# Performance work log

Hardware: AMD Instinct MI355X
Metric: run time of the kernel (lower is better)

The kernel has to match this reference:

```python
import jax, jax.numpy as jnp
import numpy as np

NUM_HEADS = 8
NUM_UNITS = 512


def setup_inputs() -> dict:
    key = jax.random.key(0)
    ks = jax.random.split(key, 5)
    B, S, D = 2, 4096, NUM_UNITS
    scale = 1.0 / np.sqrt(D)
    return {
        "x": jax.random.normal(ks[0], (B, S, D), dtype=jnp.float32),
        "Wq": jax.random.normal(ks[1], (D, NUM_UNITS), dtype=jnp.float32) * scale,
        "Wk": jax.random.normal(ks[2], (D, NUM_UNITS), dtype=jnp.float32) * scale,
        "Wv": jax.random.normal(ks[3], (D, NUM_UNITS), dtype=jnp.float32) * scale,
        "Wo": jax.random.normal(ks[4], (D, NUM_UNITS), dtype=jnp.float32) * scale,
    }


def reference(x, Wq, Wk, Wv, Wo):
    B, S, _ = x.shape
    H = NUM_HEADS
    Dh = NUM_UNITS // H

    # QKV linear projections (self-attention: K_V = (x, x))
    Q = x @ Wq  # [B,S,U]
    K = x @ Wk
    V = x @ Wv

    # split heads -> [B,H,S,Dh]
    def split(t):
        return t.reshape(B, S, H, Dh).transpose(0, 2, 1, 3)

    Qh, Kh, Vh = split(Q), split(K), split(V)

    # scaled dot-product attention, bias = 0, no mask, no dropout (training=False)
    scores = jnp.einsum("bhqd,bhkd->bhqk", Qh, Kh) / jnp.sqrt(
        jnp.asarray(Dh, dtype=x.dtype)
    )
    attn = jax.nn.softmax(scores, axis=-1)
    ctx = jnp.einsum("bhqk,bhkd->bhqd", attn, Vh)

    # combine heads -> [B,S,U], then output projection
    ctx = ctx.transpose(0, 2, 1, 3).reshape(B, S, NUM_UNITS)
    return ctx @ Wo
```

## Files before the change

kernel.cpp:

```cpp
#include <hip/hip_runtime.h>

typedef __attribute__((ext_vector_type(8))) short short8;
typedef __attribute__((ext_vector_type(4))) float f32x4;
typedef __attribute__((ext_vector_type(4))) unsigned short us4;
typedef unsigned short ushort_t;
typedef unsigned int uint_t;

typedef const __attribute__((address_space(1))) void* gas1;
typedef __attribute__((address_space(3))) void* las3;

#define LDS_FENCE()                                            \
  do {                                                         \
    asm volatile("s_waitcnt lgkmcnt(0)" ::: "memory");         \
    __builtin_amdgcn_sched_barrier(0);                         \
  } while (0)

__device__ __forceinline__ ushort_t f2b(float f) {
  union { float f; uint_t u; } v; v.f = f;
  return (ushort_t)((v.u + 0x7fffu + ((v.u >> 16) & 1u)) >> 16);
}

__device__ __forceinline__ uint_t cvtpk(float lo, float hi) {
  uint_t r;
  asm("v_cvt_pk_bf16_f32 %0, %1, %2" : "=v"(r) : "v"(lo), "v"(hi));
  return r;
}

__device__ __forceinline__ void gld_lds16(const ushort_t* g, void* l) {
  __builtin_amdgcn_global_load_lds((gas1)g, (las3)l, 16, 0, 0);
}

__global__ void cvt_x_kernel(const float* __restrict__ x, ushort_t* __restrict__ xb, int n4) {
  int i = blockIdx.x * blockDim.x + threadIdx.x;
  if (i >= n4) return;
  float4 v = ((const float4*)x)[i];
  ushort4 o;
  o.x = f2b(v.x); o.y = f2b(v.y); o.z = f2b(v.z); o.w = f2b(v.w);
  ((ushort4*)xb)[i] = o;
}

__global__ void cvt_wt_kernel(const float* __restrict__ W0, const float* __restrict__ W1,
                              const float* __restrict__ W2, const float* __restrict__ W3,
                              ushort_t* __restrict__ T0, ushort_t* __restrict__ T1,
                              ushort_t* __restrict__ T2, ushort_t* __restrict__ T3) {
  const float* W; ushort_t* T;
  switch (blockIdx.z) {
    case 0: W = W0; T = T0; break;
    case 1: W = W1; T = T1; break;
    case 2: W = W2; T = T2; break;
    default: W = W3; T = T3; break;
  }
  __shared__ ushort_t Tl[64 * 68];
  int t = threadIdx.x;
  int kt = blockIdx.x & 7, nt = blockIdx.x >> 3;
  int krow = t >> 4;
  int ncol = (t & 15) * 4;
#pragma unroll
  for (int j = 0; j < 4; ++j) {
    int k = j * 16 + krow;
    float4 v = *(const float4*)&W[(size_t)(kt * 64 + k) * 512 + nt * 64 + ncol];
    const float* vf = (const float*)&v;
#pragma unroll
    for (int e = 0; e < 4; ++e)
      Tl[(ncol + e) * 68 + k] = f2b(vf[e]);
  }
  __syncthreads();
#pragma unroll
  for (int j = 0; j < 4; ++j) {
    int f = j * 1024 + t * 4;
    int n = f >> 6, k = f & 63;
    *(ushort4*)&T[(size_t)(nt * 64 + n) * 512 + kt * 64 + k] =
        *(const ushort4*)&Tl[n * 68 + k];
  }
}

__global__ __launch_bounds__(256) void gemm_qkv_kernel(
    const ushort_t* __restrict__ A,
    const ushort_t* __restrict__ WqT, const ushort_t* __restrict__ WkT,
    const ushort_t* __restrict__ WvT,
    ushort_t* __restrict__ Qo, ushort_t* __restrict__ Ko, ushort_t* __restrict__ VTo) {
  const int K = 512, N = 512, S = 4096;
  const ushort_t* BT; ushort_t* out; int mode;
  switch (blockIdx.z) {
    case 0: BT = WqT; out = Qo;  mode = 0; break;
    case 1: BT = WkT; out = Ko;  mode = 0; break;
    default: BT = WvT; out = VTo; mode = 1; break;
  }
  __shared__ ushort_t Al[128 * 64];
  __shared__ ushort_t Bl[128 * 64];

  int tid = threadIdx.x, lane = tid & 63, w = tid >> 6;
  int g = lane >> 4, ln = lane & 15;
  int wr = w >> 1, wc = w & 1;
  int m0 = blockIdx.y * 128;
  int n0 = blockIdx.x * 128;

  f32x4 acc[4][4];
  const f32x4 zz = {0.f, 0.f, 0.f, 0.f};
#pragma unroll
  for (int i = 0; i < 4; ++i)
#pragma unroll
    for (int j = 0; j < 4; ++j) acc[i][j] = zz;

  for (int kt = 0; kt < 8; ++kt) {
    __syncthreads();
#pragma unroll
    for (int i = 0; i < 4; ++i) {
      int p = i * 256 + tid, row = p >> 3, sl = p & 7, sp = sl ^ (row & 7);
      gld_lds16(A + (size_t)(m0 + row) * K + kt * 64 + sp * 8,
                (char*)Al + (i * 256 + (tid & 192)) * 16);
    }
#pragma unroll
    for (int i = 0; i < 4; ++i) {
      int p = i * 256 + tid, row = p >> 3, sl = p & 7, sp = sl ^ (row & 7);
      gld_lds16(BT + (size_t)(n0 + row) * K + kt * 64 + sp * 8,
                (char*)Bl + (i * 256 + (tid & 192)) * 16);
    }
    __syncthreads();

#pragma unroll
    for (int kc = 0; kc < 2; ++kc) {
      short8 af[4], bf[4];
#pragma unroll
      for (int mt = 0; mt < 4; ++mt) {
        int row = wr * 64 + mt * 16 + ln;
        af[mt] = *(const short8*)((char*)Al + row * 128 + (((kc * 4 + g) ^ (row & 7)) * 16));
      }
#pragma unroll
      for (int nt = 0; nt < 4; ++nt) {
        int row = wc * 64 + nt * 16 + ln;
        bf[nt] = *(const short8*)((char*)Bl + row * 128 + (((kc * 4 + g) ^ (row & 7)) * 16));
      }
#pragma unroll
      for (int mt = 0; mt < 4; ++mt)
#pragma unroll
        for (int nt = 0; nt < 4; ++nt)
          acc[mt][nt] = __builtin_amdgcn_mfma_f32_16x16x32_bf16(af[mt], bf[nt], acc[mt][nt], 0, 0, 0);
    }
  }

  if (mode == 0) {
#pragma unroll
    for (int mt = 0; mt < 4; ++mt)
#pragma unroll
      for (int nt = 0; nt < 4; ++nt)
#pragma unroll
        for (int jj = 0; jj < 4; ++jj) {
          int m = m0 + wr * 64 + mt * 16 + 4 * g + jj;
          int n = n0 + wc * 64 + nt * 16 + ln;
          out[(size_t)m * N + n] = f2b(acc[mt][nt][jj]);
        }
  } else {
#pragma unroll
    for (int mt = 0; mt < 4; ++mt)
#pragma unroll
      for (int nt = 0; nt < 4; ++nt) {
        int s0 = m0 + wr * 64 + mt * 16 + 4 * g;
        int u = n0 + wc * 64 + nt * 16 + ln;
        int b = s0 >> 12, s = s0 & 4095;
        int h = u >> 6, d = u & 63;
        us4 pv;
#pragma unroll
        for (int jj = 0; jj < 4; ++jj) pv[jj] = f2b(acc[mt][nt][jj]);
        *(us4*)&VTo[((size_t)((b * 8 + h) * 64 + d)) * S + s] = pv;
      }
  }
}

__global__ __launch_bounds__(256) void gemm_ao_kernel(
    const ushort_t* __restrict__ A, const ushort_t* __restrict__ BT,
    float* __restrict__ out) {
  const int K = 512, N = 512;
  __shared__ ushort_t Al[128 * 64];
  __shared__ ushort_t Bl[128 * 64];

  int tid = threadIdx.x, lane = tid & 63, w = tid >> 6;
  int g = lane >> 4, ln = lane & 15;
  int wr = w >> 1, wc = w & 1;
  int m0 = blockIdx.y * 128;
  int n0 = blockIdx.x * 128;

  f32x4 acc[4][4];
  const f32x4 zz = {0.f, 0.f, 0.f, 0.f};
#pragma unroll
  for (int i = 0; i < 4; ++i)
#pragma unroll
    for (int j = 0; j < 4; ++j) acc[i][j] = zz;

  for (int kt = 0; kt < 8; ++kt) {
    __syncthreads();
#pragma unroll
    for (int i = 0; i < 4; ++i) {
      int p = i * 256 + tid, row = p >> 3, sl = p & 7, sp = sl ^ (row & 7);
      gld_lds16(A + (size_t)(m0 + row) * K + kt * 64 + sp * 8,
                (char*)Al + (i * 256 + (tid & 192)) * 16);
    }
#pragma unroll
    for (int i = 0; i < 4; ++i) {
      int p = i * 256 + tid, row = p >> 3, sl = p & 7, sp = sl ^ (row & 7);
      gld_lds16(BT + (size_t)(n0 + row) * K + kt * 64 + sp * 8,
                (char*)Bl + (i * 256 + (tid & 192)) * 16);
    }
    __syncthreads();

#pragma unroll
    for (int kc = 0; kc < 2; ++kc) {
      short8 af[4], bf[4];
#pragma unroll
      for (int mt = 0; mt < 4; ++mt) {
        int row = wr * 64 + mt * 16 + ln;
        af[mt] = *(const short8*)((char*)Al + row * 128 + (((kc * 4 + g) ^ (row & 7)) * 16));
      }
#pragma unroll
      for (int nt = 0; nt < 4; ++nt) {
        int row = wc * 64 + nt * 16 + ln;
        bf[nt] = *(const short8*)((char*)Bl + row * 128 + (((kc * 4 + g) ^ (row & 7)) * 16));
      }
#pragma unroll
      for (int mt = 0; mt < 4; ++mt)
#pragma unroll
        for (int nt = 0; nt < 4; ++nt)
          acc[mt][nt] = __builtin_amdgcn_mfma_f32_16x16x32_bf16(af[mt], bf[nt], acc[mt][nt], 0, 0, 0);
    }
  }
#pragma unroll
  for (int mt = 0; mt < 4; ++mt)
#pragma unroll
    for (int nt = 0; nt < 4; ++nt)
#pragma unroll
      for (int jj = 0; jj < 4; ++jj) {
        int m = m0 + wr * 64 + mt * 16 + 4 * g + jj;
        int n = n0 + wc * 64 + nt * 16 + ln;
        out[(size_t)m * N + n] = acc[mt][nt][jj];
      }
}

__global__ __launch_bounds__(256) void attn_kernel(
    const ushort_t* __restrict__ Qg, const ushort_t* __restrict__ Kg,
    const ushort_t* __restrict__ VTg, ushort_t* __restrict__ CTXg) {
  const int S = 4096, U = 512, DH = 64;
  const float CSC = 0.125f * 1.44269504089f;
  int qb = blockIdx.x, h = blockIdx.y, b = blockIdx.z;
  int tid = threadIdx.x, lane = tid & 63, w = tid >> 6;
  int g = lane >> 4, ln = lane & 15;

  __shared__ ushort_t Kl[64 * 64];
  __shared__ ushort_t Vl[64 * 64];
  __shared__ ushort_t Pl[4][16 * 72];

  const ushort_t* qp = Qg + ((size_t)b * S + qb * 64 + w * 16 + ln) * U + h * DH + g * 8;
  short8 qf0 = *(const short8*)qp;
  short8 qf1 = *(const short8*)(qp + 32);

  f32x4 acc[4];
  const f32x4 zz = {0.f, 0.f, 0.f, 0.f};
#pragma unroll
  for (int i = 0; i < 4; ++i) acc[i] = zz;
  float mrun = -INFINITY, lrun = 0.f;

  int r = tid >> 3;
  int c8 = (tid & 7) * 8;
  const ushort_t* kbase = Kg + ((size_t)b * S + r) * U + h * DH + c8;
  const ushort_t* vbase = VTg + ((size_t)((b * 8 + h) * 64 + r)) * S + c8;

  for (int it = 0; it < 64; ++it) {
    int kv0 = it * 64;
    uint4 k1 = *(const uint4*)(kbase + (size_t)kv0 * U);
    uint4 k2 = *(const uint4*)(kbase + (size_t)(kv0 + 32) * U);
    uint4 v1 = *(const uint4*)(vbase + kv0);
    uint4 v2 = *(const uint4*)(vbase + (size_t)32 * S + kv0);
    __syncthreads();
    {
      int by1 = (r * 128 + c8 * 2) ^ ((r & 7) << 4);
      *(uint4*)((char*)Kl + by1) = k1;
      *(uint4*)((char*)Vl + by1) = v1;
      int r2 = r + 32;
      int by2 = (r2 * 128 + c8 * 2) ^ ((r2 & 7) << 4);
      *(uint4*)((char*)Kl + by2) = k2;
      *(uint4*)((char*)Vl + by2) = v2;
    }
    __syncthreads();

    f32x4 st[4];
#pragma unroll
    for (int m = 0; m < 4; ++m) {
      int row = m * 16 + ln;
      short8 kf0 = *(const short8*)((char*)Kl + ((row * 128 + 16 * g) ^ ((row & 7) << 4)));
      short8 kf1 = *(const short8*)((char*)Kl + ((row * 128 + 64 + 16 * g) ^ ((row & 7) << 4)));
      st[m] = __builtin_amdgcn_mfma_f32_16x16x32_bf16(kf0, qf0, zz, 0, 0, 0);
      st[m] = __builtin_amdgcn_mfma_f32_16x16x32_bf16(kf1, qf1, st[m], 0, 0, 0);
    }

    float mx0 = fmaxf(fmaxf(st[0][0], st[0][1]), fmaxf(st[0][2], st[0][3]));
    float mx1 = fmaxf(fmaxf(st[1][0], st[1][1]), fmaxf(st[1][2], st[1][3]));
    float mx2 = fmaxf(fmaxf(st[2][0], st[2][1]), fmaxf(st[2][2], st[2][3]));
    float mx3 = fmaxf(fmaxf(st[3][0], st[3][1]), fmaxf(st[3][2], st[3][3]));
    float smax = fmaxf(fmaxf(mx0, mx1), fmaxf(mx2, mx3));
    smax = fmaxf(smax, __shfl_xor(smax, 16));
    smax = fmaxf(smax, __shfl_xor(smax, 32));
    float tmax = smax * CSC;

    float mnew = fmaxf(mrun, tmax);
    if (!__all(tmax <= mrun + 8.0f)) {
      float alpha = __builtin_amdgcn_exp2f(mrun - mnew);
      mrun = mnew;
      lrun *= alpha;
      float av[4];
#pragma unroll
      for (int jj = 0; jj < 4; ++jj) av[jj] = __shfl(alpha, 4 * g + jj);
#pragma unroll
      for (int dt = 0; dt < 4; ++dt)
#pragma unroll
        for (int jj = 0; jj < 4; ++jj) acc[dt][jj] *= av[jj];
    }

    float nb = -mrun;
    float p[16];
    float ps = 0.f;
#pragma unroll
    for (int m = 0; m < 4; ++m)
#pragma unroll
      for (int jj = 0; jj < 4; ++jj) {
        float y = __builtin_amdgcn_exp2f(__builtin_fmaf(st[m][jj], CSC, nb));
        p[m * 4 + jj] = y;
        ps += y;
      }
    ps += __shfl_xor(ps, 16);
    ps += __shfl_xor(ps, 32);
    lrun += ps;

#pragma unroll
    for (int m = 0; m < 4; ++m) {
      uint2 pv;
      pv.x = cvtpk(p[m * 4 + 0], p[m * 4 + 1]);
      pv.y = cvtpk(p[m * 4 + 2], p[m * 4 + 3]);
      *(uint2*)&Pl[w][ln * 72 + m * 16 + 4 * g] = pv;
    }
    LDS_FENCE();

#pragma unroll
    for (int c = 0; c < 2; ++c) {
      short8 pf = *(const short8*)&Pl[w][ln * 72 + 32 * c + 8 * g];
#pragma unroll
      for (int dt = 0; dt < 4; ++dt) {
        int row = dt * 16 + ln;
        short8 vf = *(const short8*)((char*)Vl + ((row * 128 + 64 * c + 16 * g) ^ ((row & 7) << 4)));
        acc[dt] = __builtin_amdgcn_mfma_f32_16x16x32_bf16(pf, vf, acc[dt], 0, 0, 0);
      }
    }
  }

  float inv_l = 1.f / lrun;
  float lv[4];
#pragma unroll
  for (int jj = 0; jj < 4; ++jj) lv[jj] = __shfl(inv_l, 4 * g + jj);
#pragma unroll
  for (int dt = 0; dt < 4; ++dt)
#pragma unroll
    for (int jj = 0; jj < 4; ++jj) {
      int s = qb * 64 + w * 16 + 4 * g + jj;
      int u = h * 64 + dt * 16 + ln;
      CTXg[((size_t)b * S + s) * U + u] = f2b(acc[dt][jj] * lv[jj]);
    }
}

extern "C" void kernel_launch(void* const* d_in, const int* in_sizes, int n_in,
                              void* d_out, int out_size, void* d_ws, size_t ws_size,
                              hipStream_t stream) {
  const float* x  = (const float*)d_in[0];
  const float* Wq = (const float*)d_in[1];
  const float* Wk = (const float*)d_in[2];
  const float* Wv = (const float*)d_in[3];
  const float* Wo = (const float*)d_in[4];
  float* out = (float*)d_out;

  ushort_t* ws  = (ushort_t*)d_ws;
  ushort_t* xb  = ws;
  ushort_t* WqT = xb + 4194304;
  ushort_t* WkT = WqT + 262144;
  ushort_t* WvT = WkT + 262144;
  ushort_t* WoT = WvT + 262144;
  ushort_t* Qb  = WoT + 262144;
  ushort_t* Kb  = Qb + 4194304;
  ushort_t* VTb = Kb + 4194304;
  ushort_t* CTX = xb;

  cvt_x_kernel<<<4096, 256, 0, stream>>>(x, xb, 1048576);
  cvt_wt_kernel<<<dim3(64, 1, 4), 256, 0, stream>>>(Wq, Wk, Wv, Wo, WqT, WkT, WvT, WoT);
  gemm_qkv_kernel<<<dim3(4, 64, 3), 256, 0, stream>>>(xb, WqT, WkT, WvT, Qb, Kb, VTb);
  attn_kernel<<<dim3(64, 8, 2), 256, 0, stream>>>(Qb, Kb, VTb, CTX);
  gemm_ao_kernel<<<dim3(4, 64), 256, 0, stream>>>(CTX, WoT, out);
}
```

Measured before the change: 250.0 us.

## Split attention KV range across two blocks and merge partials in a combine kernel

The attention kernel now splits the key/value sequence into parts (two when workspace allows), with each block handling half the KV tiles. Each block writes a normalized partial output plus a log-sum-exp value, and a new combine kernel merges the partials into the context buffer. This doubles the grid from 1024 to 2048 blocks to raise occupancy on a GPU with many CUs, at the cost of an extra kernel launch, extra partial-output traffic, and an extra bf16 rounding of the partials. The row-max reduction is also regrouped into three-input max operations.

```diff
diff --git a/kernel.cpp b/kernel.cpp
--- a/kernel.cpp
+++ b/kernel.cpp
@@ -20,6 +20,11 @@
   return (ushort_t)((v.u + 0x7fffu + ((v.u >> 16) & 1u)) >> 16);
 }
 
+__device__ __forceinline__ float b2f(ushort_t u) {
+  union { uint_t u; float f; } v; v.u = ((uint_t)u) << 16;
+  return v.f;
+}
+
 __device__ __forceinline__ uint_t cvtpk(float lo, float hi) {
   uint_t r;
   asm("v_cvt_pk_bf16_f32 %0, %1, %2" : "=v"(r) : "v"(lo), "v"(hi));
@@ -28,6 +33,10 @@
 
 __device__ __forceinline__ void gld_lds16(const ushort_t* g, void* l) {
   __builtin_amdgcn_global_load_lds((gas1)g, (las3)l, 16, 0, 0);
+}
+
+__device__ __forceinline__ float max3f(float a, float b, float c) {
+  return fmaxf(fmaxf(a, b), c);
 }
 
 __global__ void cvt_x_kernel(const float* __restrict__ x, ushort_t* __restrict__ xb, int n4) {
@@ -237,10 +246,13 @@
 
 __global__ __launch_bounds__(256) void attn_kernel(
     const ushort_t* __restrict__ Qg, const ushort_t* __restrict__ Kg,
-    const ushort_t* __restrict__ VTg, ushort_t* __restrict__ CTXg) {
+    const ushort_t* __restrict__ VTg, ushort_t* __restrict__ Obuf,
+    float* __restrict__ Lbuf, int ntiles) {
   const int S = 4096, U = 512, DH = 64;
   const float CSC = 0.125f * 1.44269504089f;
-  int qb = blockIdx.x, h = blockIdx.y, b = blockIdx.z;
+  int qb = blockIdx.x, h = blockIdx.y;
+  int b = blockIdx.z & 1, part = blockIdx.z >> 1;
+  int bh = b * 8 + h;
   int tid = threadIdx.x, lane = tid & 63, w = tid >> 6;
   int g = lane >> 4, ln = lane & 15;
 
@@ -261,10 +273,11 @@
   int r = tid >> 3;
   int c8 = (tid & 7) * 8;
   const ushort_t* kbase = Kg + ((size_t)b * S + r) * U + h * DH + c8;
-  const ushort_t* vbase = VTg + ((size_t)((b * 8 + h) * 64 + r)) * S + c8;
-
-  for (int it = 0; it < 64; ++it) {
-    int kv0 = it * 64;
+  const ushort_t* vbase = VTg + ((size_t)(bh * 64 + r)) * S + c8;
+
+  int it0 = part * ntiles;
+  for (int ii = 0; ii < ntiles; ++ii) {
+    int kv0 = (it0 + ii) * 64;
     uint4 k1 = *(const uint4*)(kbase + (size_t)kv0 * U);
     uint4 k2 = *(const uint4*)(kbase + (size_t)(kv0 + 32) * U);
     uint4 v1 = *(const uint4*)(vbase + kv0);
@@ -291,11 +304,12 @@
       st[m] = __builtin_amdgcn_mfma_f32_16x16x32_bf16(kf1, qf1, st[m], 0, 0, 0);
     }
 
-    float mx0 = fmaxf(fmaxf(st[0][0], st[0][1]), fmaxf(st[0][2], st[0][3]));
-    float mx1 = fmaxf(fmaxf(st[1][0], st[1][1]), fmaxf(st[1][2], st[1][3]));
-    float mx2 = fmaxf(fmaxf(st[2][0], st[2][1]), fmaxf(st[2][2], st[2][3]));
-    float mx3 = fmaxf(fmaxf(st[3][0], st[3][1]), fmaxf(st[3][2], st[3][3]));
-    float smax = fmaxf(fmaxf(mx0, mx1), fmaxf(mx2, mx3));
+    float t0 = max3f(st[0][0], st[0][1], st[0][2]);
+    float t1 = max3f(st[0][3], st[1][0], st[1][1]);
+    float t2 = max3f(st[1][2], st[1][3], st[2][0]);
+    float t3 = max3f(st[2][1], st[2][2], st[2][3]);
+    float t4 = max3f(st[3][0], st[3][1], st[3][2]);
+    float smax = fmaxf(max3f(t0, t1, t2), max3f(t3, t4, st[3][3]));
     smax = fmaxf(smax, __shfl_xor(smax, 16));
     smax = fmaxf(smax, __shfl_xor(smax, 32));
     float tmax = smax * CSC;
@@ -354,14 +368,58 @@
   float lv[4];
 #pragma unroll
   for (int jj = 0; jj < 4; ++jj) lv[jj] = __shfl(inv_l, 4 * g + jj);
+  ushort_t* ob = Obuf + (size_t)part * 4194304 + ((size_t)bh * S) * 64;
 #pragma unroll
   for (int dt = 0; dt < 4; ++dt)
 #pragma unroll
     for (int jj = 0; jj < 4; ++jj) {
       int s = qb * 64 + w * 16 + 4 * g + jj;
-      int u = h * 64 + dt * 16 + ln;
-      CTXg[((size_t)b * S + s) * U + u] = f2b(acc[dt][jj] * lv[jj]);
-    }
+      int d = dt * 16 + ln;
+      ob[(size_t)s * 64 + d] = f2b(acc[dt][jj] * lv[jj]);
+    }
+  if (g == 0) {
+    int s = qb * 64 + w * 16 + ln;
+    Lbuf[part * 65536 + bh * S + s] = mrun + __log2f(lrun);
+  }
+}
+
+__global__ void combine_kernel(const ushort_t* __restrict__ Obuf,
+                               const float* __restrict__ Lbuf,
+                               ushort_t* __restrict__ CTX, int nparts) {
+  int tid = threadIdx.x;
+  int row = blockIdx.x * 32 + (tid >> 3);
+  int c = (tid & 7) * 8;
+  int bh = row >> 12, s = row & 4095;
+  int b = bh >> 3, h = bh & 7;
+
+  us4 n0a = *(const us4*)&Obuf[(size_t)row * 64 + c];
+  us4 n0b = *(const us4*)&Obuf[(size_t)row * 64 + c + 4];
+  float o[8];
+  if (nparts == 2) {
+    float L0 = Lbuf[row];
+    float L1 = Lbuf[65536 + row];
+    us4 n1a = *(const us4*)&Obuf[(size_t)(4194304 + row * 64) + c];
+    us4 n1b = *(const us4*)&Obuf[(size_t)(4194304 + row * 64) + c + 4];
+    float Lm = fmaxf(L0, L1);
+    float w0 = __builtin_amdgcn_exp2f(L0 - Lm);
+    float w1 = __builtin_amdgcn_exp2f(L1 - Lm);
+    float inv = 1.f / (w0 + w1);
+    float a0 = w0 * inv, a1 = w1 * inv;
+#pragma unroll
+    for (int j = 0; j < 4; ++j) {
+      o[j]     = a0 * b2f(n0a[j]) + a1 * b2f(n1a[j]);
+      o[j + 4] = a0 * b2f(n0b[j]) + a1 * b2f(n1b[j]);
+    }
+  } else {
+#pragma unroll
+    for (int j = 0; j < 4; ++j) { o[j] = b2f(n0a[j]); o[j + 4] = b2f(n0b[j]); }
+  }
+  us4 w0v, w1v;
+#pragma unroll
+  for (int j = 0; j < 4; ++j) { w0v[j] = f2b(o[j]); w1v[j] = f2b(o[j + 4]); }
+  ushort_t* dst = &CTX[((size_t)(b * 4096 + s)) * 512 + h * 64 + c];
+  *(us4*)dst = w0v;
+  *(us4*)(dst + 4) = w1v;
 }
 
 extern "C" void kernel_launch(void* const* d_in, const int* in_sizes, int n_in,
@@ -383,11 +441,17 @@
   ushort_t* Qb  = WoT + 262144;
   ushort_t* Kb  = Qb + 4194304;
   ushort_t* VTb = Kb + 4194304;
+  ushort_t* Obuf = VTb + 4194304;
   ushort_t* CTX = xb;
+
+  int nparts = (ws_size >= 52953088u) ? 2 : 1;
+  float* Lbuf = (float*)(Obuf + (size_t)nparts * 4194304);
+  int ntiles = 64 / nparts;
 
   cvt_x_kernel<<<4096, 256, 0, stream>>>(x, xb, 1048576);
   cvt_wt_kernel<<<dim3(64, 1, 4), 256, 0, stream>>>(Wq, Wk, Wv, Wo, WqT, WkT, WvT, WoT);
   gemm_qkv_kernel<<<dim3(4, 64, 3), 256, 0, stream>>>(xb, WqT, WkT, WvT, Qb, Kb, VTb);
-  attn_kernel<<<dim3(64, 8, 2), 256, 0, stream>>>(Qb, Kb, VTb, CTX);
+  attn_kernel<<<dim3(64, 8, 2 * nparts), 256, 0, stream>>>(Qb, Kb, VTb, Obuf, Lbuf, ntiles);
+  combine_kernel<<<2048, 256, 0, stream>>>(Obuf, Lbuf, CTX, nparts);
   gemm_ao_kernel<<<dim3(4, 64), 256, 0, stream>>>(CTX, WoT, out);
 }
```

Measured after the change: 249.4 us. Within noise of the previous version (-0.3%).
